# Performance work log

Hardware: AMD Instinct MI355X
Metric: run time of the kernel (lower is better)

## Reference

```python
import jax, jax.numpy as jnp
import numpy as np

# norse LIFParameters defaults with v_th overridden to 0.23
DT = 1e-3
TAU_SYN_INV = 200.0   # 1/5e-3
TAU_MEM_INV = 100.0   # 1/1e-2
V_TH = 0.23
ENC_V_TH = 1.0        # encoder uses default LIFParameters (v_th=1.0)
SEQ_LEN = 24
HIDDEN = 256
N_CLASSES = 10


def heaviside(x):
    return (x > 0).astype(x.dtype)


def encode(x):
    """ConstantCurrentLIFEncoder: lif_current_encoder over SEQ_LEN steps. x: [B, F] -> [T, B, F] spikes."""
    def step(v, _):
        v = v + DT * TAU_MEM_INV * (x - v)          # dv = dt*tau_mem_inv*((v_leak - v) + I)
        z = heaviside(v - ENC_V_TH)
        v = (1.0 - z) * v                            # reset to v_reset = 0
        return v, z
    _, zs = jax.lax.scan(step, jnp.zeros_like(x), None, length=SEQ_LEN)
    return zs


def lif_ff_step(inp, v, i):
    """norse lif_feed_forward_step: decay v with old i, decay i, spike, reset, then add input to i."""
    v_dec = v + DT * TAU_MEM_INV * (i - v)           # v_leak = 0
    i_dec = i * (1.0 - DT * TAU_SYN_INV)
    z = heaviside(v_dec - V_TH)
    v_new = (1.0 - z) * v_dec                        # v_reset = 0
    i_new = i_dec + inp
    return z, v_new, i_new


def setup_inputs() -> dict:
    key = jax.random.key(0)
    ks = jax.random.split(key, 8)
    B, F = 4096, 1024
    def lin(k, fan_in, fan_out):
        bound = 1.0 / np.sqrt(fan_in)
        kw, kb = jax.random.split(k)
        W = jax.random.uniform(kw, (fan_out, fan_in), jnp.float32, -bound, bound)
        b = jax.random.uniform(kb, (fan_out,), jnp.float32, -bound, bound)
        return W, b
    x = jax.random.normal(ks[0], (B, F), jnp.float32)
    W1, b1 = lin(ks[1], F, HIDDEN)
    W2, b2 = lin(ks[2], HIDDEN, HIDDEN)
    W3, b3 = lin(ks[3], HIDDEN, HIDDEN)
    Wli = jax.random.normal(ks[4], (N_CLASSES, HIDDEN), jnp.float32) * np.sqrt(2.0 / HIDDEN)
    return {"x": x, "W1": W1, "b1": b1, "W2": W2, "b2": b2, "W3": W3, "b3": b3, "Wli": Wli}


def reference(x, W1, b1, W2, b2, W3, b3, Wli):
    # dropout layers are identity in eval mode
    enc = encode(x)                                   # [T, B, F]
    B = x.shape[0]
    z2 = lambda d: jnp.zeros((B, d), x.dtype)
    carry0 = (z2(HIDDEN), z2(HIDDEN), z2(HIDDEN), z2(HIDDEN), z2(HIDDEN), z2(HIDDEN),
              z2(N_CLASSES), z2(N_CLASSES))
    def step(c, z):
        v1, i1, v2, i2, v3, i3, vo, io = c
        o1, v1, i1 = lif_ff_step(z @ W1.T + b1, v1, i1)
        o2, v2, i2 = lif_ff_step(o1 @ W2.T + b2, v2, i2)
        o2 = o2 + o1                                  # residual
        o3, v3, i3 = lif_ff_step(o2 @ W3.T + b3, v3, i3)
        o3 = o3 + o2                                  # residual
        # LILinearCell li_step: v from old i, i decays then accumulates W @ input (no bias)
        vo = vo + DT * TAU_MEM_INV * (io - vo)
        io = io * (1.0 - DT * TAU_SYN_INV) + o3 @ Wli.T
        return (v1, i1, v2, i2, v3, i3, vo, io), vo
    _, voltages = jax.lax.scan(step, carry0, enc)     # [T, B, n_classes]
    return voltages[-1]                               # decode = last timestep
```

## Files before the change

kernel.cpp:

```cpp
#include <hip/hip_runtime.h>
#include <hip/hip_bf16.h>

#define FEAT   1024
#define HID    256
#define TSTEPS 24
#define NCLS   10

typedef unsigned int u32;
typedef unsigned long long u64;
typedef unsigned short u16;
typedef float v2f __attribute__((ext_vector_type(2)));

constexpr int OFF_W1T  = 0;
constexpr int OFF_W2T  = OFF_W1T + 1025*HID;
constexpr int OFF_W3T  = OFF_W2T + 257*HID;
constexpr int OFF_WLI  = OFF_W3T + 257*HID;
constexpr int OFF_B1   = OFF_WLI + NCLS*HID;
constexpr int OFF_B2   = OFF_B1 + HID;
constexpr int OFF_B3   = OFF_B2 + HID;

constexpr u32 ZPAD1 = 1024u << 10;
constexpr u32 ZPAD2 = 256u  << 10;

struct CoefT { float c[TSTEPS]; };
constexpr CoefT make_coef() {
    CoefT r{};
    double c = 0.0, p9 = 1.0;
    r.c[TSTEPS-1] = 0.0f;
    for (int u = TSTEPS-1; u > 0; u--) {
        c = 0.8 * c + 0.1 * p9;
        p9 *= 0.9;
        r.c[u-1] = (float)c;
    }
    return r;
}
__device__ constexpr CoefT COEF = make_coef();

__device__ __forceinline__ u32 detect_bf16(const void* __restrict__ x, u32 lane) {
    float v = __bfloat162float(((const __hip_bfloat16*)x)[lane]);
    u64 bad = __ballot(!(fabsf(v) < 100.0f));
    return bad == 0ull ? 1u : 0u;
}

__device__ __forceinline__ float rd_any(const void* p, int idx, u32 isbf) {
    return isbf ? __bfloat162float(((const __hip_bfloat16*)p)[idx])
                : ((const float*)p)[idx];
}

__device__ __forceinline__ float4 rd4(const void* p, int i, u32 isbf) {
    if (isbf) {
        const u32* q = (const u32*)p;
        u32 a = q[i >> 1], b = q[(i >> 1) + 1];
        float4 r;
        r.x = __uint_as_float(a << 16); r.y = __uint_as_float(a & 0xffff0000u);
        r.z = __uint_as_float(b << 16); r.w = __uint_as_float(b & 0xffff0000u);
        return r;
    }
    return ((const float4*)p)[i >> 2];
}

__global__ __launch_bounds__(256) void prep_k(const void* __restrict__ x,
        const void* W1, const void* W2, const void* W3, const void* Wli,
        const void* b1, const void* b2, const void* b3, float* __restrict__ ws) {
    const u32 isbf = detect_bf16(x, threadIdx.x & 63);
    const u32 t = threadIdx.x;
    int b = blockIdx.x;

    if (b == 384) {
        for (u32 e = t; e < NCLS*HID; e += 256) ws[OFF_WLI + e] = rd_any(Wli, e, isbf);
        ws[OFF_B1 + t] = rd_any(b1, t, isbf);
        ws[OFF_B2 + t] = rd_any(b2, t, isbf);
        ws[OFF_B3 + t] = rd_any(b3, t, isbf);
        ws[OFF_W1T + 1024*HID + t] = 0.f;
        ws[OFF_W2T + 256*HID + t] = 0.f;
        ws[OFF_W3T + 256*HID + t] = 0.f;
        return;
    }

    const void* src; float* dst; int srcW, h0, f0;
    if (b < 256)      { src = W1; dst = ws + OFF_W1T; srcW = FEAT; h0 = (b >> 5) * 32; f0 = (b & 31) * 32; }
    else if (b < 320) { int tb = b - 256; src = W2; dst = ws + OFF_W2T; srcW = HID; h0 = (tb >> 3) * 32; f0 = (tb & 7) * 32; }
    else              { int tb = b - 320; src = W3; dst = ws + OFF_W3T; srcW = HID; h0 = (tb >> 3) * 32; f0 = (tb & 7) * 32; }

    __shared__ float sm[32 * 36];
    {
        u32 r = t >> 3, c4 = (t & 7) * 4;
        float4 w = rd4(src, (h0 + r) * srcW + f0 + c4, isbf);
        *(float4*)&sm[r * 36 + c4] = w;
    }
    __syncthreads();
    {
        u32 f = t >> 3, h4 = (t & 7) * 4;
        float4 o;
        o.x = sm[(h4 + 0) * 36 + f];
        o.y = sm[(h4 + 1) * 36 + f];
        o.z = sm[(h4 + 2) * 36 + f];
        o.w = sm[(h4 + 3) * 36 + f];
        *(float4*)&dst[(size_t)(f0 + f) * HID + h0 + h4] = o;
    }
}

__device__ __forceinline__ u32 mbcnt64(u64 m) {
    return __builtin_amdgcn_mbcnt_hi((u32)(m >> 32),
           __builtin_amdgcn_mbcnt_lo((u32)m, 0u));
}
__device__ __forceinline__ u32 round8(u32 n) { return (n + 7u) & ~7u; }


__device__ __forceinline__ u32 build_listE(u32* list, u32 lm, u32 lane) {
    u32 cnt = (u32)__builtin_popcount(lm);
    u32 pos = 0, n = 0;
    #pragma unroll
    for (int b = 0; b < 5; b++) {
        u64 B = __ballot(((cnt >> b) & 1u) != 0);
        pos += mbcnt64(B) << b;
        n += ((u32)__builtin_popcountll(B)) << b;
    }
    while (lm) {
        u32 j = (u32)__builtin_ctz(lm); lm &= lm - 1;
        list[pos++] = ((lane << 4) + j) << 10;
    }
    u32 np = round8(n);
    if (lane < np - n) list[n + lane] = ZPAD1;
    return np;
}

__device__ __forceinline__ u32 build_listZ(u32* list, u32 lm, u32 start, u32 lane) {
    u32 cnt = (u32)__builtin_popcount(lm);
    u64 B0 = __ballot((cnt & 1u) != 0);
    u64 B1 = __ballot((cnt & 2u) != 0);
    u64 B2 = __ballot((cnt & 4u) != 0);
    u32 pos = start + mbcnt64(B0) + 2u*mbcnt64(B1) + 4u*mbcnt64(B2);
    u32 n = start + (u32)__builtin_popcountll(B0) + 2u*(u32)__builtin_popcountll(B1)
          + 4u*(u32)__builtin_popcountll(B2);
    while (lm) {
        u32 j = (u32)__builtin_ctz(lm); lm &= lm - 1;
        list[pos++] = ((lane << 2) + j) << 10;
    }
    u32 np = round8(n);
    if (lane < np - n) list[n + lane] = ZPAD2;
    return np;
}

__device__ __forceinline__ void gather(v2f& A, v2f& B, const float* __restrict__ Wt,
                                       const u32* __restrict__ list, u32 np, u32 lane16) {
    const char* __restrict__ base = (const char*)Wt;
    const uint4* lp = (const uint4*)list;
    u32 nch = np >> 3;
    for (u32 c = 0; c < nch; c++) {
        uint4 d0 = lp[2*c], d1 = lp[2*c + 1];
        u32 a0 = d0.x + lane16, a1 = d0.y + lane16, a2 = d0.z + lane16, a3 = d0.w + lane16;
        u32 a4 = d1.x + lane16, a5 = d1.y + lane16, a6 = d1.z + lane16, a7 = d1.w + lane16;
        const float4 w0 = *(const float4*)(base + a0);
        const float4 w1 = *(const float4*)(base + a1);
        const float4 w2 = *(const float4*)(base + a2);
        const float4 w3 = *(const float4*)(base + a3);
        const float4 w4 = *(const float4*)(base + a4);
        const float4 w5 = *(const float4*)(base + a5);
        const float4 w6 = *(const float4*)(base + a6);
        const float4 w7 = *(const float4*)(base + a7);
        A += (v2f){w0.x, w0.y}; B += (v2f){w0.z, w0.w};
        A += (v2f){w1.x, w1.y}; B += (v2f){w1.z, w1.w};
        A += (v2f){w2.x, w2.y}; B += (v2f){w2.z, w2.w};
        A += (v2f){w3.x, w3.y}; B += (v2f){w3.z, w3.w};
        A += (v2f){w4.x, w4.y}; B += (v2f){w4.z, w4.w};
        A += (v2f){w5.x, w5.y}; B += (v2f){w5.z, w5.w};
        A += (v2f){w6.x, w6.y}; B += (v2f){w6.z, w6.w};
        A += (v2f){w7.x, w7.y}; B += (v2f){w7.z, w7.w};
    }
}

__global__ __launch_bounds__(256) void snn_k(const void* __restrict__ xin,
                                             const float* __restrict__ ws,
                                             void* __restrict__ out) {
    const u32 tid  = threadIdx.x;
    const u32 lane = tid & 63;
    const u32 wv   = tid >> 6;
    const int row  = blockIdx.x * 4 + wv;
    const u32 lane16 = lane * 16;
    const u32 isbf = detect_bf16(xin, lane);

    const float* __restrict__ W1T = ws + OFF_W1T;
    const float* __restrict__ W2T = ws + OFF_W2T;
    const float* __restrict__ W3T = ws + OFF_W3T;
    const float* __restrict__ WLI = ws + OFF_WLI;

    __shared__ u32 sched[12 * 256];
    __shared__ __align__(16) u32 listE[4][1032];
    __shared__ __align__(16) u32 listL[4][528];

    {
        float xv[16];
        if (isbf) {
            const uint4* xp = (const uint4*)((const u16*)xin + (size_t)row*FEAT + lane*16);
            uint4 A = xp[0], B = xp[1];
            u32 w[8] = {A.x, A.y, A.z, A.w, B.x, B.y, B.z, B.w};
            #pragma unroll
            for (int i = 0; i < 8; i++) {
                xv[2*i]   = __uint_as_float(w[i] << 16);
                xv[2*i+1] = __uint_as_float(w[i] & 0xffff0000u);
            }
        } else {
            const float4* xp = (const float4*)((const float*)xin + (size_t)row*FEAT + lane*16);
            float4 A = xp[0], B = xp[1], C = xp[2], D = xp[3];
            float tmp[16] = {A.x,A.y,A.z,A.w,B.x,B.y,B.z,B.w,C.x,C.y,C.z,C.w,D.x,D.y,D.z,D.w};
            #pragma unroll
            for (int i = 0; i < 16; i++) xv[i] = tmp[i];
        }
        u32 smreg[12];
        #pragma unroll
        for (int i = 0; i < 12; i++) smreg[i] = 0;
        #pragma unroll
        for (int j = 0; j < 16; j++) {
            float v = 0.f;
            #pragma unroll
            for (int t = 0; t < TSTEPS; t++) {
                v = v + 0.1f * (xv[j] - v);
                bool z = v > 1.0f;
                v = z ? 0.0f : v;
                if (z) smreg[t >> 1] |= 1u << (((t & 1) << 4) + j);
            }
        }
        #pragma unroll
        for (int i = 0; i < 12; i++) sched[i * 256 + tid] = smreg[i];
    }

    float v1[4], i1[4], v2[4], i2[4], v3[4], i3[4], g[4];
    #pragma unroll
    for (int k = 0; k < 4; k++) {
        v1[k]=0.f; i1[k]=0.f; v2[k]=0.f; i2[k]=0.f; v3[k]=0.f; i3[k]=0.f; g[k]=0.f;
    }
    const u32 lane4 = lane * 4;
    const float4 b1v = *(const float4*)(ws + OFF_B1 + lane4);
    const float4 b2v = *(const float4*)(ws + OFF_B2 + lane4);
    const float4 b3v = *(const float4*)(ws + OFF_B3 + lane4);

    u32* const lE = listE[wv];
    u32* const lL = listL[wv];

    u32 pairreg = 0;
    for (int t = 0; t < TSTEPS; t++) {
        if ((t & 1) == 0) pairreg = sched[(t >> 1) * 256 + tid];
        const u32 lmE = (t & 1) ? (pairreg >> 16) : (pairreg & 0xffffu);

        u32 nE = build_listE(lE, lmE, lane);
        v2f accA = {b1v.x, b1v.y}, accB = {b1v.z, b1v.w};
        gather(accA, accB, W1T, lE, nE, lane16);
        float a1[4] = {accA.x, accA.y, accB.x, accB.y};

        float o1v[4]; u32 lm1 = 0;
        #pragma unroll
        for (int kk = 0; kk < 4; kk++) {
            float vd = v1[kk] + 0.1f * (i1[kk] - v1[kk]);
            i1[kk] = i1[kk] * 0.8f;
            bool z = vd > 0.23f;
            v1[kk] = z ? 0.0f : vd;
            i1[kk] = i1[kk] + a1[kk];
            o1v[kk] = z ? 1.0f : 0.0f;
            lm1 |= (z ? 1u : 0u) << kk;
        }

        u32 n1p = build_listZ(lL, lm1, 0u, lane);
        accA = (v2f){b2v.x, b2v.y}; accB = (v2f){b2v.z, b2v.w};
        gather(accA, accB, W2T, lL, n1p, lane16);
        float a2[4] = {accA.x, accA.y, accB.x, accB.y};

        float o2v[4]; u32 lm2 = 0;
        #pragma unroll
        for (int kk = 0; kk < 4; kk++) {
            float vd = v2[kk] + 0.1f * (i2[kk] - v2[kk]);
            i2[kk] = i2[kk] * 0.8f;
            bool z = vd > 0.23f;
            v2[kk] = z ? 0.0f : vd;
            i2[kk] = i2[kk] + a2[kk];
            o2v[kk] = (z ? 1.0f : 0.0f) + o1v[kk];
            lm2 |= (z ? 1u : 0u) << kk;
        }

        u32 nend = build_listZ(lL, lm2, n1p, lane);
        accA = (v2f){b3v.x, b3v.y}; accB = (v2f){b3v.z, b3v.w};
        gather(accA, accB, W3T, lL, nend, lane16);
        float a3[4] = {accA.x, accA.y, accB.x, accB.y};

        const float cf = COEF.c[t];
        #pragma unroll
        for (int kk = 0; kk < 4; kk++) {
            float vd = v3[kk] + 0.1f * (i3[kk] - v3[kk]);
            i3[kk] = i3[kk] * 0.8f;
            bool z = vd > 0.23f;
            v3[kk] = z ? 0.0f : vd;
            i3[kk] = i3[kk] + a3[kk];
            float o3 = (z ? 1.0f : 0.0f) + o2v[kk];
            g[kk] += cf * o3;
        }
    }

    float s[NCLS];
    #pragma unroll
    for (int c = 0; c < NCLS; c++) {
        const float4 w = *(const float4*)(WLI + c*HID + lane4);
        float p = g[0]*w.x + g[1]*w.y + g[2]*w.z + g[3]*w.w;
        #pragma unroll
        for (int d = 32; d > 0; d >>= 1) p += __shfl_xor(p, d, 64);
        s[c] = p;
    }
    if (lane == 0) {
        if (isbf) {
            __hip_bfloat16* o = (__hip_bfloat16*)out + (size_t)row*NCLS;
            #pragma unroll
            for (int c = 0; c < NCLS; c++) o[c] = __float2bfloat16(s[c]);
        } else {
            float* o = (float*)out + (size_t)row*NCLS;
            #pragma unroll
            for (int c = 0; c < NCLS; c++) o[c] = s[c];
        }
    }
}

extern "C" void kernel_launch(void* const* d_in, const int* in_sizes, int n_in,
                              void* d_out, int out_size, void* d_ws, size_t ws_size,
                              hipStream_t stream) {
    const void* x   = d_in[0];
    const void* W1  = d_in[1];
    const void* b1  = d_in[2];
    const void* W2  = d_in[3];
    const void* b2  = d_in[4];
    const void* W3  = d_in[5];
    const void* b3  = d_in[6];
    const void* Wli = d_in[7];
    float* ws = (float*)d_ws;
    const int batch = in_sizes[0] / FEAT;

    prep_k<<<385, 256, 0, stream>>>(x, W1, W2, W3, Wli, b1, b2, b3, ws);
    snn_k<<<batch/4, 256, 0, stream>>>(x, ws, d_out);
}
```

Before: 165.4 us.

## Use 16-bit spike index lists, 16-wide gather unroll, and early layer-3 partial gather

Spike index lists in LDS now hold 16-bit row indices instead of pre-shifted 32-bit byte offsets, which halves LDS footprint and list traffic. The row shift is now done in the gather loop. The gather loop now issues 16 independent float4 weight loads per iteration instead of 8, to keep more memory requests in flight. Layer 3's contribution from layer-1 spikes is gathered right after the layer-2 gather, so only the layer-2 spike part remains after layer 2 finishes. Lists are padded to multiples of 16 with zero-row indices, so small spike counts cost more wasted padding loads.

```diff
diff --git a/kernel.cpp b/kernel.cpp
--- a/kernel.cpp
+++ b/kernel.cpp
@@ -18,9 +18,6 @@
 constexpr int OFF_B1   = OFF_WLI + NCLS*HID;
 constexpr int OFF_B2   = OFF_B1 + HID;
 constexpr int OFF_B3   = OFF_B2 + HID;
-
-constexpr u32 ZPAD1 = 1024u << 10;
-constexpr u32 ZPAD2 = 256u  << 10;
 
 struct CoefT { float c[TSTEPS]; };
 constexpr CoefT make_coef() {
@@ -104,10 +101,9 @@
     return __builtin_amdgcn_mbcnt_hi((u32)(m >> 32),
            __builtin_amdgcn_mbcnt_lo((u32)m, 0u));
 }
-__device__ __forceinline__ u32 round8(u32 n) { return (n + 7u) & ~7u; }
-
-
-__device__ __forceinline__ u32 build_listE(u32* list, u32 lm, u32 lane) {
+
+
+__device__ __forceinline__ u32 build_listE(u16* list, u32 lm, u32 lane) {
     u32 cnt = (u32)__builtin_popcount(lm);
     u32 pos = 0, n = 0;
     #pragma unroll
@@ -118,14 +114,14 @@
     }
     while (lm) {
         u32 j = (u32)__builtin_ctz(lm); lm &= lm - 1;
-        list[pos++] = ((lane << 4) + j) << 10;
-    }
-    u32 np = round8(n);
-    if (lane < np - n) list[n + lane] = ZPAD1;
+        list[pos++] = (u16)((lane << 4) + j);
+    }
+    u32 np = (n + 15u) & ~15u;
+    if (lane < np - n) list[n + lane] = (u16)1024;
     return np;
 }
 
-__device__ __forceinline__ u32 build_listZ(u32* list, u32 lm, u32 start, u32 lane) {
+__device__ __forceinline__ u32 build_listZ(u16* list, u32 lm, u32 start, u32 lane) {
     u32 cnt = (u32)__builtin_popcount(lm);
     u64 B0 = __ballot((cnt & 1u) != 0);
     u64 B1 = __ballot((cnt & 2u) != 0);
@@ -135,38 +131,32 @@
           + 4u*(u32)__builtin_popcountll(B2);
     while (lm) {
         u32 j = (u32)__builtin_ctz(lm); lm &= lm - 1;
-        list[pos++] = ((lane << 2) + j) << 10;
-    }
-    u32 np = round8(n);
-    if (lane < np - n) list[n + lane] = ZPAD2;
+        list[pos++] = (u16)((lane << 2) + j);
+    }
+    u32 np = (n + 15u) & ~15u;
+    if (lane < np - n) list[n + lane] = (u16)256;
     return np;
 }
 
-__device__ __forceinline__ void gather(v2f& A, v2f& B, const float* __restrict__ Wt,
-                                       const u32* __restrict__ list, u32 np, u32 lane16) {
+__device__ __forceinline__ void gather16(v2f& A, v2f& B, const float* __restrict__ Wt,
+                                         const u16* __restrict__ list, u32 np, u32 lane16) {
     const char* __restrict__ base = (const char*)Wt;
-    const uint4* lp = (const uint4*)list;
-    u32 nch = np >> 3;
-    for (u32 c = 0; c < nch; c++) {
-        uint4 d0 = lp[2*c], d1 = lp[2*c + 1];
-        u32 a0 = d0.x + lane16, a1 = d0.y + lane16, a2 = d0.z + lane16, a3 = d0.w + lane16;
-        u32 a4 = d1.x + lane16, a5 = d1.y + lane16, a6 = d1.z + lane16, a7 = d1.w + lane16;
-        const float4 w0 = *(const float4*)(base + a0);
-        const float4 w1 = *(const float4*)(base + a1);
-        const float4 w2 = *(const float4*)(base + a2);
-        const float4 w3 = *(const float4*)(base + a3);
-        const float4 w4 = *(const float4*)(base + a4);
-        const float4 w5 = *(const float4*)(base + a5);
-        const float4 w6 = *(const float4*)(base + a6);
-        const float4 w7 = *(const float4*)(base + a7);
-        A += (v2f){w0.x, w0.y}; B += (v2f){w0.z, w0.w};
-        A += (v2f){w1.x, w1.y}; B += (v2f){w1.z, w1.w};
-        A += (v2f){w2.x, w2.y}; B += (v2f){w2.z, w2.w};
-        A += (v2f){w3.x, w3.y}; B += (v2f){w3.z, w3.w};
-        A += (v2f){w4.x, w4.y}; B += (v2f){w4.z, w4.w};
-        A += (v2f){w5.x, w5.y}; B += (v2f){w5.z, w5.w};
-        A += (v2f){w6.x, w6.y}; B += (v2f){w6.z, w6.w};
-        A += (v2f){w7.x, w7.y}; B += (v2f){w7.z, w7.w};
+    for (u32 c = 0; c < np; c += 16) {
+        uint4 d0 = *(const uint4*)(list + c);
+        uint4 d1 = *(const uint4*)(list + c + 8);
+        u32 w[8] = {d0.x, d0.y, d0.z, d0.w, d1.x, d1.y, d1.z, d1.w};
+        float4 v[16];
+        #pragma unroll
+        for (int i = 0; i < 8; i++) {
+            u32 lo = w[i] & 0xffffu, hi = w[i] >> 16;
+            v[2*i]   = *(const float4*)(base + (lo << 10) + lane16);
+            v[2*i+1] = *(const float4*)(base + (hi << 10) + lane16);
+        }
+        #pragma unroll
+        for (int i = 0; i < 16; i++) {
+            A += (v2f){v[i].x, v[i].y};
+            B += (v2f){v[i].z, v[i].w};
+        }
     }
 }
 
@@ -186,8 +176,8 @@
     const float* __restrict__ WLI = ws + OFF_WLI;
 
     __shared__ u32 sched[12 * 256];
-    __shared__ __align__(16) u32 listE[4][1032];
-    __shared__ __align__(16) u32 listL[4][528];
+    __shared__ __align__(16) u16 listE[4][1024];
+    __shared__ __align__(16) u16 listL[4][512];
 
     {
         float xv[16];
@@ -235,17 +225,17 @@
     const float4 b2v = *(const float4*)(ws + OFF_B2 + lane4);
     const float4 b3v = *(const float4*)(ws + OFF_B3 + lane4);
 
-    u32* const lE = listE[wv];
-    u32* const lL = listL[wv];
+    u16* const lE = listE[wv];
+    u16* const lL = listL[wv];
 
     u32 pairreg = 0;
     for (int t = 0; t < TSTEPS; t++) {
         if ((t & 1) == 0) pairreg = sched[(t >> 1) * 256 + tid];
         const u32 lmE = (t & 1) ? (pairreg >> 16) : (pairreg & 0xffffu);
 
-        u32 nE = build_listE(lE, lmE, lane);
+        u32 npE = build_listE(lE, lmE, lane);
         v2f accA = {b1v.x, b1v.y}, accB = {b1v.z, b1v.w};
-        gather(accA, accB, W1T, lE, nE, lane16);
+        gather16(accA, accB, W1T, lE, npE, lane16);
         float a1[4] = {accA.x, accA.y, accB.x, accB.y};
 
         float o1v[4]; u32 lm1 = 0;
@@ -260,9 +250,11 @@
             lm1 |= (z ? 1u : 0u) << kk;
         }
 
-        u32 n1p = build_listZ(lL, lm1, 0u, lane);
+        u32 np1 = build_listZ(lL, lm1, 0u, lane);
         accA = (v2f){b2v.x, b2v.y}; accB = (v2f){b2v.z, b2v.w};
-        gather(accA, accB, W2T, lL, n1p, lane16);
+        gather16(accA, accB, W2T, lL, np1, lane16);
+        v2f acc3A = {b3v.x, b3v.y}, acc3B = {b3v.z, b3v.w};
+        gather16(acc3A, acc3B, W3T, lL, np1, lane16);
         float a2[4] = {accA.x, accA.y, accB.x, accB.y};
 
         float o2v[4]; u32 lm2 = 0;
@@ -277,10 +269,9 @@
             lm2 |= (z ? 1u : 0u) << kk;
         }
 
-        u32 nend = build_listZ(lL, lm2, n1p, lane);
-        accA = (v2f){b3v.x, b3v.y}; accB = (v2f){b3v.z, b3v.w};
-        gather(accA, accB, W3T, lL, nend, lane16);
-        float a3[4] = {accA.x, accA.y, accB.x, accB.y};
+        u32 np2 = build_listZ(lL, lm2, np1, lane);
+        gather16(acc3A, acc3B, W3T, lL + np1, np2 - np1, lane16);
+        float a3[4] = {acc3A.x, acc3A.y, acc3B.x, acc3B.y};
 
         const float cf = COEF.c[t];
         #pragma unroll
```

Measured after the change: 184.2 us. +11.4%, slower.
